# Kernel tuning notes

Measured on AMD Instinct MI355X. Metric: run time of the kernel, lower is better.

The kernel has to match this reference:

```python
import jax, jax.numpy as jnp
import numpy as np

EPS = 1e-12  # matches torch F.normalize eps

def _l2norm(x, axis):
    n = jnp.sqrt(jnp.sum(x * x, axis=axis, keepdims=True))
    return x / jnp.maximum(n, EPS)

def setup_inputs() -> dict:
    key = jax.random.key(0)
    k1, k2, k3, k4 = jax.random.split(key, 4)
    b, n_way, k_shot, q, c, h, w = 2, 5, 5, 75, 64, 21, 21
    return {
        "support_xf": jax.random.normal(k1, (b, n_way * k_shot, c, h, w), dtype=jnp.float32),
        "support_y": jax.random.randint(k2, (b, n_way * k_shot), 0, n_way),
        "query_xf": jax.random.normal(k3, (b, q, c, h, w), dtype=jnp.float32),
        "query_y": jax.random.randint(k4, (b, q), 0, n_way),
        "n_way": n_way,
        "k_shot": k_shot,
    }

def reference(support_xf, support_y, query_xf, query_y, n_way, k_shot):
    b, q, c, h, w = query_xf.shape
    hw = h * w
    # k_shot averaging: (b, n_way, k_shot, c, h, w) -> mean over shots -> (b, n_way, c, hw)
    sup = support_xf.reshape(b, n_way, k_shot, c, hw).mean(axis=2)
    qry = query_xf.reshape(b, q, c, hw)
    # cosine similarity: L2-normalize each local descriptor along channel dim
    sup_n = _l2norm(sup, axis=2)  # (b, n_way, c, hw_s)
    qry_n = _l2norm(qry, axis=2)  # (b, q, c, hw_q)
    # inner product matrix: (b, q, n_way, hw_q, hw_s)
    sim = jnp.einsum('bqcm,bwcn->bqwmn', qry_n, sup_n)
    # topk with k=1 along support descriptors, mean over k == max
    topv = jnp.max(sim, axis=-1)  # (b, q, n_way, hw_q)
    logits = topv.sum(axis=-1).reshape(b * q, n_way)  # image-to-class score
    return logits
```

## Files before the change

### kernel.cpp

```cpp
#include <hip/hip_runtime.h>
#include <hip/hip_bf16.h>

namespace {
constexpr int kB = 2, kW = 5, kS = 5, kQ = 75, kC = 64, kHW = 441;
constexpr int kNP = 448;
constexpr int kMP = 448;
constexpr int kCHUNK = 112;
constexpr int kLDT = 65;
constexpr int kTiles = kB * kQ * kW;
constexpr int kThreads = 448;
constexpr int kWaves = 7;
constexpr int kPrepGrid = 8 * 81;

typedef short bf16x8 __attribute__((ext_vector_type(8)));
typedef float f32x16 __attribute__((ext_vector_type(16)));
typedef __attribute__((address_space(3))) unsigned int lds_u32;
typedef const __attribute__((address_space(1))) unsigned int gbl_u32;
}

__global__ __launch_bounds__(256) void prep_k(const float* __restrict__ sup,
                                              const float* __restrict__ qry,
                                              unsigned short* __restrict__ snT,
                                              unsigned short* __restrict__ qnT) {
  __shared__ float img_t[kCHUNK * kLDT];
  __shared__ float inv[kCHUNK];
  const int tid = threadIdx.x;
  const int x = blockIdx.x & 7;
  const int j = blockIdx.x >> 3;

  const int start0 = (x < 6) ? 94 * x : 564 + 93 * (x - 6);
  const int start1 = (x + 1 < 6) ? 94 * (x + 1) : 564 + 93 * (x + 1 - 6);
  const int lo = (start0 + 4) / 5, hi = (start1 + 4) / 5;
  const int cnt = hi - lo;
  const int nq = 4 * cnt;

  bool is_sup;
  int bw = 0, bq = 0, chunk;
  if (j < nq) {
    is_sup = false;
    bq = lo + (j >> 2);
    chunk = j & 3;
  } else {
    int js = j - nq;
    if (js >= 5) return;
    is_sup = true;
    int u = x + 8 * js;
    bw = u >> 2;
    chunk = u & 3;
  }

  const int m0 = chunk * kCHUNK;
  const int mcnt = min(kCHUNK, kHW - m0);
  unsigned short* dst;

  if (is_sup) {
    const float* base = sup + (size_t)bw * kS * kC * kHW;
    for (int i = tid; i < kC * kCHUNK; i += 256) {
      int c = i / kCHUNK, mm = i % kCHUNK;
      float v = 0.f;
      if (mm < mcnt) {
        const float* p = base + (size_t)c * kHW + m0 + mm;
        float s = 0.f;
#pragma unroll
        for (int k = 0; k < kS; ++k) s += p[(size_t)k * kC * kHW];
        v = s * (1.f / kS);
      }
      img_t[mm * kLDT + c] = v;
    }
    dst = snT + (size_t)bw * kNP * kC;
  } else {
    const float* base = qry + (size_t)bq * kC * kHW;
    for (int i = tid; i < kC * kCHUNK; i += 256) {
      int c = i / kCHUNK, mm = i % kCHUNK;
      img_t[mm * kLDT + c] = (mm < mcnt) ? base[(size_t)c * kHW + m0 + mm] : 0.f;
    }
    dst = qnT + (size_t)bq * kMP * kC;
  }
  __syncthreads();

  if (tid < kCHUNK) {
    float ss = 0.f;
#pragma unroll
    for (int c = 0; c < kC; ++c) { float v = img_t[tid * kLDT + c]; ss += v * v; }
    inv[tid] = 1.f / fmaxf(sqrtf(ss), 1e-12f);
  }
  __syncthreads();

  for (int i8 = tid; i8 < kCHUNK * 8; i8 += 256) {
    int m = i8 >> 3, c8 = (i8 & 7) * 8;
    float sc = inv[m];
    union { unsigned short u[8]; uint4 v; } pk;
#pragma unroll
    for (int jj = 0; jj < 8; ++jj) {
      __hip_bfloat16 o = __float2bfloat16(img_t[m * kLDT + c8 + jj] * sc);
      pk.u[jj] = *reinterpret_cast<unsigned short*>(&o);
    }
    *reinterpret_cast<uint4*>(dst + ((size_t)(m0 + m) * kC + c8)) = pk.v;
  }
}

__device__ __forceinline__ float max16_v(const f32x16& a) {
  float m0 = fmaxf(fmaxf(a[0], a[1]), a[2]);
  float m1 = fmaxf(fmaxf(a[3], a[4]), a[5]);
  float m2 = fmaxf(fmaxf(a[6], a[7]), a[8]);
  float m3 = fmaxf(fmaxf(a[9], a[10]), a[11]);
  float m4 = fmaxf(fmaxf(a[12], a[13]), a[14]);
  return fmaxf(fmaxf(fmaxf(m0, m1), m2), fmaxf(fmaxf(m3, m4), a[15]));
}
__device__ __forceinline__ float max12_v(const f32x16& a) {
  float m0 = fmaxf(fmaxf(a[0], a[1]), a[2]);
  float m1 = fmaxf(fmaxf(a[3], a[4]), a[5]);
  float m2 = fmaxf(fmaxf(a[6], a[7]), a[8]);
  float m3 = fmaxf(fmaxf(a[9], a[10]), a[11]);
  return fmaxf(fmaxf(m0, m1), fmaxf(m2, m3));
}

__global__ __launch_bounds__(kThreads) void dn4_main_k(const unsigned short* __restrict__ qnT,
                                                       const unsigned short* __restrict__ snT,
                                                       float* __restrict__ out) {
  __shared__ __align__(16) unsigned short As[kNP * kC];
  __shared__ float part[kWaves];
  const int tid = threadIdx.x;

  const int xcd = blockIdx.x & 7, jj = blockIdx.x >> 3;
  const int idx = (xcd < 6) ? xcd * 94 + jj : 564 + (xcd - 6) * 93 + jj;

  const int w = idx % kW;
  const int bq = idx / kW;
  const int b = bq / kQ;

  const int lane = tid & 63;
  const int lh = lane >> 5;
  const int lm = lane & 31;
  const int wid = tid >> 6;
  const int ct0 = wid * 2;

  const unsigned short* sb = snT + (size_t)(b * kW + w) * kNP * kC;
  const unsigned short* qb = qnT + (size_t)bq * kMP * kC;
  const char* sbase = (const char*)sb;

  bf16x8 bf[2][4];
#pragma unroll
  for (int ct = 0; ct < 2; ++ct) {
    int m = (ct0 + ct) * 32 + lm;
#pragma unroll
    for (int kk = 0; kk < 4; ++kk)
      bf[ct][kk] = *reinterpret_cast<const bf16x8*>(qb + (size_t)m * kC + kk * 16 + lh * 8);
  }

#pragma unroll
  for (int it = 0; it < 8; ++it) {
    int L = it * kThreads + tid;
    int srcj = (L & ~7) | ((L & 7) ^ ((L >> 3) & 7));
    __builtin_amdgcn_global_load_lds((gbl_u32*)(sbase + ((size_t)srcj << 4)),
                                     (lds_u32*)((char*)As + ((size_t)L << 4)), 16, 0, 0);
  }

  f32x16 z;
#pragma unroll
  for (int r = 0; r < 16; ++r) z[r] = 0.f;
  float rm[2] = {-INFINITY, -INFINITY};

  asm volatile("s_waitcnt vmcnt(4)" ::: "memory");
  __builtin_amdgcn_sched_barrier(0);
  __builtin_amdgcn_s_barrier();

#pragma unroll 1
  for (int nt = 0; nt < 7; ++nt) {
    bf16x8 af[4];
    int n = nt * 32 + lm;
#pragma unroll
    for (int kk = 0; kk < 4; ++kk) {
      int k16 = kk * 2 + lh;
      af[kk] = *reinterpret_cast<const bf16x8*>(As + ((size_t)(n * 8 + (k16 ^ (n & 7))) << 3));
    }
#pragma unroll
    for (int ct = 0; ct < 2; ++ct) {
      f32x16 acc = z;
#pragma unroll
      for (int kk = 0; kk < 4; ++kk)
        acc = __builtin_amdgcn_mfma_f32_32x32x16_bf16(af[kk], bf[ct][kk], acc, 0, 0, 0);
      rm[ct] = fmaxf(rm[ct], max16_v(acc));
    }
  }

  asm volatile("s_waitcnt vmcnt(0)" ::: "memory");
  __builtin_amdgcn_sched_barrier(0);
  __builtin_amdgcn_s_barrier();

#pragma unroll 1
  for (int nt = 7; nt < 13; ++nt) {
    bf16x8 af[4];
    int n = nt * 32 + lm;
#pragma unroll
    for (int kk = 0; kk < 4; ++kk) {
      int k16 = kk * 2 + lh;
      af[kk] = *reinterpret_cast<const bf16x8*>(As + ((size_t)(n * 8 + (k16 ^ (n & 7))) << 3));
    }
#pragma unroll
    for (int ct = 0; ct < 2; ++ct) {
      f32x16 acc = z;
#pragma unroll
      for (int kk = 0; kk < 4; ++kk)
        acc = __builtin_amdgcn_mfma_f32_32x32x16_bf16(af[kk], bf[ct][kk], acc, 0, 0, 0);
      rm[ct] = fmaxf(rm[ct], max16_v(acc));
    }
  }

  {
    bf16x8 af[4];
    int n = 13 * 32 + lm;
#pragma unroll
    for (int kk = 0; kk < 4; ++kk) {
      int k16 = kk * 2 + lh;
      af[kk] = *reinterpret_cast<const bf16x8*>(As + ((size_t)(n * 8 + (k16 ^ (n & 7))) << 3));
    }
#pragma unroll
    for (int ct = 0; ct < 2; ++ct) {
      f32x16 acc = z;
#pragma unroll
      for (int kk = 0; kk < 4; ++kk)
        acc = __builtin_amdgcn_mfma_f32_32x32x16_bf16(af[kk], bf[ct][kk], acc, 0, 0, 0);
      float t = max12_v(acc);
      if (lh == 0) t = fmaxf(t, acc[12]);
      rm[ct] = fmaxf(rm[ct], t);
    }
  }

  float s = fmaxf(rm[0], __shfl_xor(rm[0], 32, 64)) +
            fmaxf(rm[1], __shfl_xor(rm[1], 32, 64));
#pragma unroll
  for (int off = 1; off < 32; off <<= 1) s += __shfl_xor(s, off, 64);

  if (lane == 0) part[wid] = s;
  __syncthreads();
  if (tid == 0) {
    float t = 0.f;
#pragma unroll
    for (int v = 0; v < kWaves; ++v) t += part[v];
    out[idx] = t;
  }
}

extern "C" void kernel_launch(void* const* d_in, const int* in_sizes, int n_in,
                              void* d_out, int out_size, void* d_ws, size_t ws_size,
                              hipStream_t stream) {
  const float* sup = (const float*)d_in[0];
  const float* qry = (const float*)d_in[2];
  float* out = (float*)d_out;

  unsigned short* snT = (unsigned short*)d_ws;
  unsigned short* qnT = snT + (size_t)kB * kW * kNP * kC;

  prep_k<<<kPrepGrid, 256, 0, stream>>>(sup, qry, snT, qnT);
  dn4_main_k<<<kTiles, kThreads, 0, stream>>>(qnT, snT, out);
}
```

Measured before the change: 38.63 us.

## Use persistent 512-block grid with double-buffered LDS halves for the main kernel

The main kernel moves from one block per (query, way) tile (750 blocks) to a fixed 512-block grid. Some blocks process two tiles, chosen by an XCD-aware rank mapping. Support staging is split into two 224-row halves held in a double-buffered LDS array, and the next half (or the next tile's first half) is prefetched while the current half is computed. The aim is to cut the tail effect of the second wave of blocks and to overlap global-to-LDS loads with MFMA work. In exchange it adds barriers and imbalance, since blocks that handle two tiles set the critical path.

```diff
diff --git a/kernel.cpp b/kernel.cpp
--- a/kernel.cpp
+++ b/kernel.cpp
@@ -10,6 +10,7 @@
 constexpr int kTiles = kB * kQ * kW;
 constexpr int kThreads = 448;
 constexpr int kWaves = 7;
+constexpr int kGrid = 512;
 constexpr int kPrepGrid = 8 * 81;
 
 typedef short bf16x8 __attribute__((ext_vector_type(8)));
@@ -31,8 +32,7 @@
   const int start0 = (x < 6) ? 94 * x : 564 + 93 * (x - 6);
   const int start1 = (x + 1 < 6) ? 94 * (x + 1) : 564 + 93 * (x + 1 - 6);
   const int lo = (start0 + 4) / 5, hi = (start1 + 4) / 5;
-  const int cnt = hi - lo;
-  const int nq = 4 * cnt;
+  const int nq = 4 * (hi - lo);
 
   bool is_sup;
   int bw = 0, bq = 0, chunk;
@@ -115,19 +115,81 @@
   return fmaxf(fmaxf(m0, m1), fmaxf(m2, m3));
 }
 
+__device__ __forceinline__ void stage_half(const unsigned short* sb, int h,
+                                           unsigned short* dstbuf, int tid) {
+  const char* sbase = (const char*)sb + (size_t)h * 1792 * 16;
+#pragma unroll
+  for (int it = 0; it < 4; ++it) {
+    int L = it * kThreads + tid;
+    int srcj = (L & ~7) | ((L & 7) ^ ((L >> 3) & 7));
+    __builtin_amdgcn_global_load_lds((gbl_u32*)(sbase + ((size_t)srcj << 4)),
+                                     (lds_u32*)((char*)dstbuf + ((size_t)L << 4)), 16, 0, 0);
+  }
+}
+
+template <bool TAIL>
+__device__ __forceinline__ void compute_half7(const unsigned short* As,
+                                              const bf16x8 bf[2][4],
+                                              int lane, float rm[2]) {
+  const int lh = lane >> 5;
+  const int lm = lane & 31;
+  const unsigned short* p0 = As + ((size_t)(lm * 8 + ((0 * 2 + lh) ^ (lm & 7))) << 3);
+  const unsigned short* p1 = As + ((size_t)(lm * 8 + ((1 * 2 + lh) ^ (lm & 7))) << 3);
+  const unsigned short* p2 = As + ((size_t)(lm * 8 + ((2 * 2 + lh) ^ (lm & 7))) << 3);
+  const unsigned short* p3 = As + ((size_t)(lm * 8 + ((3 * 2 + lh) ^ (lm & 7))) << 3);
+  f32x16 z;
+#pragma unroll
+  for (int r = 0; r < 16; ++r) z[r] = 0.f;
+
+#pragma unroll 1
+  for (int sub = 0; sub < 7; ++sub) {
+    const size_t so = (size_t)sub * 32 * kC;
+    bf16x8 af[4];
+    af[0] = *reinterpret_cast<const bf16x8*>(p0 + so);
+    af[1] = *reinterpret_cast<const bf16x8*>(p1 + so);
+    af[2] = *reinterpret_cast<const bf16x8*>(p2 + so);
+    af[3] = *reinterpret_cast<const bf16x8*>(p3 + so);
+    if (!TAIL || sub < 6) {
+#pragma unroll
+      for (int ct = 0; ct < 2; ++ct) {
+        f32x16 acc = z;
+#pragma unroll
+        for (int kk = 0; kk < 4; ++kk)
+          acc = __builtin_amdgcn_mfma_f32_32x32x16_bf16(af[kk], bf[ct][kk], acc, 0, 0, 0);
+        rm[ct] = fmaxf(rm[ct], max16_v(acc));
+      }
+    } else {
+#pragma unroll
+      for (int ct = 0; ct < 2; ++ct) {
+        f32x16 acc = z;
+#pragma unroll
+        for (int kk = 0; kk < 4; ++kk)
+          acc = __builtin_amdgcn_mfma_f32_32x32x16_bf16(af[kk], bf[ct][kk], acc, 0, 0, 0);
+        float t = max12_v(acc);
+        if (lh == 0) t = fmaxf(t, acc[12]);
+        rm[ct] = fmaxf(rm[ct], t);
+      }
+    }
+  }
+}
+
 __global__ __launch_bounds__(kThreads) void dn4_main_k(const unsigned short* __restrict__ qnT,
                                                        const unsigned short* __restrict__ snT,
                                                        float* __restrict__ out) {
-  __shared__ __align__(16) unsigned short As[kNP * kC];
+  __shared__ __align__(16) unsigned short As[2][224 * kC];
   __shared__ float part[kWaves];
   const int tid = threadIdx.x;
 
-  const int xcd = blockIdx.x & 7, jj = blockIdx.x >> 3;
-  const int idx = (xcd < 6) ? xcd * 94 + jj : 564 + (xcd - 6) * 93 + jj;
-
-  const int w = idx % kW;
-  const int bq = idx / kW;
-  const int b = bq / kQ;
+  const int xcd = blockIdx.x & 7;
+  const int s = blockIdx.x >> 3;
+  const int cnt = (xcd < 6) ? 94 : 93;
+  const int base = (xcd < 6) ? 94 * xcd : 564 + 93 * (xcd - 6);
+  const int idx0 = base + s;
+  const int rank = (s < 32) ? ((s & 1) ? (s >> 1) : -1)
+                            : (((s & 1) == 0) ? 16 + ((s - 32) >> 1) : -1);
+  const bool has2 = (rank >= 0) && (64 + rank < cnt);
+  const int idx1 = has2 ? base + 64 + rank : idx0;
+  const int P = has2 ? 4 : 2;
 
   const int lane = tid & 63;
   const int lh = lane >> 5;
@@ -135,9 +197,9 @@
   const int wid = tid >> 6;
   const int ct0 = wid * 2;
 
-  const unsigned short* sb = snT + (size_t)(b * kW + w) * kNP * kC;
-  const unsigned short* qb = qnT + (size_t)bq * kMP * kC;
-  const char* sbase = (const char*)sb;
+  const unsigned short* sb0 =
+      snT + (size_t)((idx0 / (kQ * kW)) * kW + (idx0 % kW)) * kNP * kC;
+  const unsigned short* qb0 = qnT + (size_t)(idx0 / kW) * kMP * kC;
 
   bf16x8 bf[2][4];
 #pragma unroll
@@ -145,100 +207,64 @@
     int m = (ct0 + ct) * 32 + lm;
 #pragma unroll
     for (int kk = 0; kk < 4; ++kk)
-      bf[ct][kk] = *reinterpret_cast<const bf16x8*>(qb + (size_t)m * kC + kk * 16 + lh * 8);
-  }
-
-#pragma unroll
-  for (int it = 0; it < 8; ++it) {
-    int L = it * kThreads + tid;
-    int srcj = (L & ~7) | ((L & 7) ^ ((L >> 3) & 7));
-    __builtin_amdgcn_global_load_lds((gbl_u32*)(sbase + ((size_t)srcj << 4)),
-                                     (lds_u32*)((char*)As + ((size_t)L << 4)), 16, 0, 0);
-  }
-
-  f32x16 z;
-#pragma unroll
-  for (int r = 0; r < 16; ++r) z[r] = 0.f;
+      bf[ct][kk] = *reinterpret_cast<const bf16x8*>(qb0 + (size_t)m * kC + kk * 16 + lh * 8);
+  }
+  stage_half(sb0, 0, As[0], tid);
+
   float rm[2] = {-INFINITY, -INFINITY};
 
-  asm volatile("s_waitcnt vmcnt(4)" ::: "memory");
-  __builtin_amdgcn_sched_barrier(0);
-  __builtin_amdgcn_s_barrier();
-
 #pragma unroll 1
-  for (int nt = 0; nt < 7; ++nt) {
-    bf16x8 af[4];
-    int n = nt * 32 + lm;
-#pragma unroll
-    for (int kk = 0; kk < 4; ++kk) {
-      int k16 = kk * 2 + lh;
-      af[kk] = *reinterpret_cast<const bf16x8*>(As + ((size_t)(n * 8 + (k16 ^ (n & 7))) << 3));
-    }
-#pragma unroll
-    for (int ct = 0; ct < 2; ++ct) {
-      f32x16 acc = z;
-#pragma unroll
-      for (int kk = 0; kk < 4; ++kk)
-        acc = __builtin_amdgcn_mfma_f32_32x32x16_bf16(af[kk], bf[ct][kk], acc, 0, 0, 0);
-      rm[ct] = fmaxf(rm[ct], max16_v(acc));
-    }
-  }
-
-  asm volatile("s_waitcnt vmcnt(0)" ::: "memory");
-  __builtin_amdgcn_sched_barrier(0);
-  __builtin_amdgcn_s_barrier();
-
-#pragma unroll 1
-  for (int nt = 7; nt < 13; ++nt) {
-    bf16x8 af[4];
-    int n = nt * 32 + lm;
-#pragma unroll
-    for (int kk = 0; kk < 4; ++kk) {
-      int k16 = kk * 2 + lh;
-      af[kk] = *reinterpret_cast<const bf16x8*>(As + ((size_t)(n * 8 + (k16 ^ (n & 7))) << 3));
-    }
-#pragma unroll
-    for (int ct = 0; ct < 2; ++ct) {
-      f32x16 acc = z;
-#pragma unroll
-      for (int kk = 0; kk < 4; ++kk)
-        acc = __builtin_amdgcn_mfma_f32_32x32x16_bf16(af[kk], bf[ct][kk], acc, 0, 0, 0);
-      rm[ct] = fmaxf(rm[ct], max16_v(acc));
-    }
-  }
-
-  {
-    bf16x8 af[4];
-    int n = 13 * 32 + lm;
-#pragma unroll
-    for (int kk = 0; kk < 4; ++kk) {
-      int k16 = kk * 2 + lh;
-      af[kk] = *reinterpret_cast<const bf16x8*>(As + ((size_t)(n * 8 + (k16 ^ (n & 7))) << 3));
-    }
-#pragma unroll
-    for (int ct = 0; ct < 2; ++ct) {
-      f32x16 acc = z;
-#pragma unroll
-      for (int kk = 0; kk < 4; ++kk)
-        acc = __builtin_amdgcn_mfma_f32_32x32x16_bf16(af[kk], bf[ct][kk], acc, 0, 0, 0);
-      float t = max12_v(acc);
-      if (lh == 0) t = fmaxf(t, acc[12]);
-      rm[ct] = fmaxf(rm[ct], t);
-    }
-  }
-
-  float s = fmaxf(rm[0], __shfl_xor(rm[0], 32, 64)) +
-            fmaxf(rm[1], __shfl_xor(rm[1], 32, 64));
-#pragma unroll
-  for (int off = 1; off < 32; off <<= 1) s += __shfl_xor(s, off, 64);
-
-  if (lane == 0) part[wid] = s;
-  __syncthreads();
-  if (tid == 0) {
-    float t = 0.f;
-#pragma unroll
-    for (int v = 0; v < kWaves; ++v) t += part[v];
-    out[idx] = t;
+  for (int ph = 0; ph < P; ++ph) {
+    const int cur = ph & 1;
+    const int idx = (ph >> 1) ? idx1 : idx0;
+
+    if (ph == 2) {
+      const unsigned short* qb1 = qnT + (size_t)(idx1 / kW) * kMP * kC;
+#pragma unroll
+      for (int ct = 0; ct < 2; ++ct) {
+        int m = (ct0 + ct) * 32 + lm;
+#pragma unroll
+        for (int kk = 0; kk < 4; ++kk)
+          bf[ct][kk] = *reinterpret_cast<const bf16x8*>(qb1 + (size_t)m * kC + kk * 16 + lh * 8);
+      }
+    }
+
+    if (ph + 1 < P) {
+      const int nidx = ((ph + 1) >> 1) ? idx1 : idx0;
+      const unsigned short* sbn =
+          snT + (size_t)((nidx / (kQ * kW)) * kW + (nidx % kW)) * kNP * kC;
+      stage_half(sbn, (ph + 1) & 1, As[cur ^ 1], tid);
+      asm volatile("s_waitcnt vmcnt(4)" ::: "memory");
+    } else {
+      asm volatile("s_waitcnt vmcnt(0)" ::: "memory");
+    }
+    __builtin_amdgcn_sched_barrier(0);
+    __builtin_amdgcn_s_barrier();
+    __builtin_amdgcn_sched_barrier(0);
+
+    if ((ph & 1) == 0) {
+      compute_half7<false>(As[cur], bf, lane, rm);
+      __builtin_amdgcn_s_barrier();
+      __builtin_amdgcn_sched_barrier(0);
+    } else {
+      compute_half7<true>(As[cur], bf, lane, rm);
+      float sm = fmaxf(rm[0], __shfl_xor(rm[0], 32, 64)) +
+                 fmaxf(rm[1], __shfl_xor(rm[1], 32, 64));
+#pragma unroll
+      for (int off = 1; off < 32; off <<= 1) sm += __shfl_xor(sm, off, 64);
+      if (lane == 0) part[wid] = sm;
+      asm volatile("s_waitcnt lgkmcnt(0)" ::: "memory");
+      __builtin_amdgcn_sched_barrier(0);
+      __builtin_amdgcn_s_barrier();
+      __builtin_amdgcn_sched_barrier(0);
+      if (tid == 0) {
+        float t = 0.f;
+#pragma unroll
+        for (int v = 0; v < kWaves; ++v) t += part[v];
+        out[idx] = t;
+      }
+      rm[0] = -INFINITY; rm[1] = -INFINITY;
+    }
   }
 }
 
@@ -253,5 +279,5 @@
   unsigned short* qnT = snT + (size_t)kB * kW * kNP * kC;
 
   prep_k<<<kPrepGrid, 256, 0, stream>>>(sup, qry, snT, qnT);
-  dn4_main_k<<<kTiles, kThreads, 0, stream>>>(qnT, snT, out);
-}
+  dn4_main_k<<<kGrid, kThreads, 0, stream>>>(qnT, snT, out);
+}
```

Result: slower. 39.87 us (+3.2%).

## Share one support tile in LDS across four queries per block

Applied to the files above, without the earlier changes.

The main kernel is restructured so each block loads one support class image into LDS once and has four queries read it, two waves per query, instead of one block per query-class pair. This cuts redundant support loads into LDS and the block count from 750 to 190. Each wave now holds 7 query tiles in registers (28 bf16x8 fragments), which raises register pressure. The split-phase wait that overlapped the LDS fill with early compute is replaced by a full barrier, and 190 blocks may underfill the GPU's CUs.

```diff
diff --git a/kernel.cpp b/kernel.cpp
--- a/kernel.cpp
+++ b/kernel.cpp
@@ -7,10 +7,9 @@
 constexpr int kMP = 448;
 constexpr int kCHUNK = 112;
 constexpr int kLDT = 65;
-constexpr int kTiles = kB * kQ * kW;
-constexpr int kThreads = 448;
-constexpr int kWaves = 7;
 constexpr int kPrepGrid = 8 * 81;
+constexpr int kSPerBW = 19;
+constexpr int kGrid = kB * kW * kSPerBW;
 
 typedef short bf16x8 __attribute__((ext_vector_type(8)));
 typedef float f32x16 __attribute__((ext_vector_type(16)));
@@ -31,8 +30,7 @@
   const int start0 = (x < 6) ? 94 * x : 564 + 93 * (x - 6);
   const int start1 = (x + 1 < 6) ? 94 * (x + 1) : 564 + 93 * (x + 1 - 6);
   const int lo = (start0 + 4) / 5, hi = (start1 + 4) / 5;
-  const int cnt = hi - lo;
-  const int nq = 4 * cnt;
+  const int nq = 4 * (hi - lo);
 
   bool is_sup;
   int bw = 0, bq = 0, chunk;
@@ -115,58 +113,59 @@
   return fmaxf(fmaxf(m0, m1), fmaxf(m2, m3));
 }
 
-__global__ __launch_bounds__(kThreads) void dn4_main_k(const unsigned short* __restrict__ qnT,
-                                                       const unsigned short* __restrict__ snT,
-                                                       float* __restrict__ out) {
+__global__ __launch_bounds__(512) void dn4_main_k(const unsigned short* __restrict__ qnT,
+                                                  const unsigned short* __restrict__ snT,
+                                                  float* __restrict__ out) {
   __shared__ __align__(16) unsigned short As[kNP * kC];
-  __shared__ float part[kWaves];
+  __shared__ float part[8];
   const int tid = threadIdx.x;
-
-  const int xcd = blockIdx.x & 7, jj = blockIdx.x >> 3;
-  const int idx = (xcd < 6) ? xcd * 94 + jj : 564 + (xcd - 6) * 93 + jj;
-
-  const int w = idx % kW;
-  const int bq = idx / kW;
-  const int b = bq / kQ;
+  const int bid = blockIdx.x;
+
+  const int bw = bid / kSPerBW;
+  const int s = bid % kSPerBW;
+  const int b = bw / kW;
 
   const int lane = tid & 63;
   const int lh = lane >> 5;
   const int lm = lane & 31;
   const int wid = tid >> 6;
-  const int ct0 = wid * 2;
-
-  const unsigned short* sb = snT + (size_t)(b * kW + w) * kNP * kC;
-  const unsigned short* qb = qnT + (size_t)bq * kMP * kC;
+  const int qi = wid >> 1;
+  const int wp = wid & 1;
+  const int q = s * 4 + qi;
+  const bool valid = q < kQ;
+
+  const unsigned short* sb = snT + (size_t)bw * kNP * kC;
   const char* sbase = (const char*)sb;
 
-  bf16x8 bf[2][4];
-#pragma unroll
-  for (int ct = 0; ct < 2; ++ct) {
-    int m = (ct0 + ct) * 32 + lm;
-#pragma unroll
-    for (int kk = 0; kk < 4; ++kk)
-      bf[ct][kk] = *reinterpret_cast<const bf16x8*>(qb + (size_t)m * kC + kk * 16 + lh * 8);
-  }
-
-#pragma unroll
-  for (int it = 0; it < 8; ++it) {
-    int L = it * kThreads + tid;
+  bf16x8 bf[7][4];
+  if (valid) {
+    const unsigned short* qb = qnT + (size_t)(b * kQ + q) * kMP * kC;
+#pragma unroll
+    for (int ct = 0; ct < 7; ++ct) {
+      int m = (wp * 7 + ct) * 32 + lm;
+#pragma unroll
+      for (int kk = 0; kk < 4; ++kk)
+        bf[ct][kk] = *reinterpret_cast<const bf16x8*>(qb + (size_t)m * kC + kk * 16 + lh * 8);
+    }
+  }
+
+#pragma unroll
+  for (int it = 0; it < 7; ++it) {
+    int L = it * 512 + tid;
     int srcj = (L & ~7) | ((L & 7) ^ ((L >> 3) & 7));
     __builtin_amdgcn_global_load_lds((gbl_u32*)(sbase + ((size_t)srcj << 4)),
                                      (lds_u32*)((char*)As + ((size_t)L << 4)), 16, 0, 0);
   }
-
+  __syncthreads();
+
+  float rm[7] = {-INFINITY, -INFINITY, -INFINITY, -INFINITY,
+                 -INFINITY, -INFINITY, -INFINITY};
   f32x16 z;
 #pragma unroll
   for (int r = 0; r < 16; ++r) z[r] = 0.f;
-  float rm[2] = {-INFINITY, -INFINITY};
-
-  asm volatile("s_waitcnt vmcnt(4)" ::: "memory");
-  __builtin_amdgcn_sched_barrier(0);
-  __builtin_amdgcn_s_barrier();
 
 #pragma unroll 1
-  for (int nt = 0; nt < 7; ++nt) {
+  for (int nt = 0; nt < 13; ++nt) {
     bf16x8 af[4];
     int n = nt * 32 + lm;
 #pragma unroll
@@ -174,71 +173,55 @@
       int k16 = kk * 2 + lh;
       af[kk] = *reinterpret_cast<const bf16x8*>(As + ((size_t)(n * 8 + (k16 ^ (n & 7))) << 3));
     }
-#pragma unroll
-    for (int ct = 0; ct < 2; ++ct) {
-      f32x16 acc = z;
-#pragma unroll
-      for (int kk = 0; kk < 4; ++kk)
-        acc = __builtin_amdgcn_mfma_f32_32x32x16_bf16(af[kk], bf[ct][kk], acc, 0, 0, 0);
-      rm[ct] = fmaxf(rm[ct], max16_v(acc));
-    }
-  }
-
-  asm volatile("s_waitcnt vmcnt(0)" ::: "memory");
-  __builtin_amdgcn_sched_barrier(0);
-  __builtin_amdgcn_s_barrier();
-
-#pragma unroll 1
-  for (int nt = 7; nt < 13; ++nt) {
+    if (valid) {
+#pragma unroll
+      for (int ct = 0; ct < 7; ++ct) {
+        f32x16 acc = z;
+#pragma unroll
+        for (int kk = 0; kk < 4; ++kk)
+          acc = __builtin_amdgcn_mfma_f32_32x32x16_bf16(af[kk], bf[ct][kk], acc, 0, 0, 0);
+        rm[ct] = fmaxf(rm[ct], max16_v(acc));
+      }
+    }
+  }
+
+  {
     bf16x8 af[4];
-    int n = nt * 32 + lm;
+    int n = 13 * 32 + lm;
 #pragma unroll
     for (int kk = 0; kk < 4; ++kk) {
       int k16 = kk * 2 + lh;
       af[kk] = *reinterpret_cast<const bf16x8*>(As + ((size_t)(n * 8 + (k16 ^ (n & 7))) << 3));
     }
-#pragma unroll
-    for (int ct = 0; ct < 2; ++ct) {
-      f32x16 acc = z;
-#pragma unroll
-      for (int kk = 0; kk < 4; ++kk)
-        acc = __builtin_amdgcn_mfma_f32_32x32x16_bf16(af[kk], bf[ct][kk], acc, 0, 0, 0);
-      rm[ct] = fmaxf(rm[ct], max16_v(acc));
-    }
-  }
-
-  {
-    bf16x8 af[4];
-    int n = 13 * 32 + lm;
-#pragma unroll
-    for (int kk = 0; kk < 4; ++kk) {
-      int k16 = kk * 2 + lh;
-      af[kk] = *reinterpret_cast<const bf16x8*>(As + ((size_t)(n * 8 + (k16 ^ (n & 7))) << 3));
-    }
-#pragma unroll
-    for (int ct = 0; ct < 2; ++ct) {
-      f32x16 acc = z;
-#pragma unroll
-      for (int kk = 0; kk < 4; ++kk)
-        acc = __builtin_amdgcn_mfma_f32_32x32x16_bf16(af[kk], bf[ct][kk], acc, 0, 0, 0);
-      float t = max12_v(acc);
-      if (lh == 0) t = fmaxf(t, acc[12]);
-      rm[ct] = fmaxf(rm[ct], t);
-    }
-  }
-
-  float s = fmaxf(rm[0], __shfl_xor(rm[0], 32, 64)) +
-            fmaxf(rm[1], __shfl_xor(rm[1], 32, 64));
-#pragma unroll
-  for (int off = 1; off < 32; off <<= 1) s += __shfl_xor(s, off, 64);
-
-  if (lane == 0) part[wid] = s;
-  __syncthreads();
-  if (tid == 0) {
-    float t = 0.f;
-#pragma unroll
-    for (int v = 0; v < kWaves; ++v) t += part[v];
-    out[idx] = t;
+    if (valid) {
+#pragma unroll
+      for (int ct = 0; ct < 7; ++ct) {
+        f32x16 acc = z;
+#pragma unroll
+        for (int kk = 0; kk < 4; ++kk)
+          acc = __builtin_amdgcn_mfma_f32_32x32x16_bf16(af[kk], bf[ct][kk], acc, 0, 0, 0);
+        float t = max12_v(acc);
+        if (lh == 0) t = fmaxf(t, acc[12]);
+        rm[ct] = fmaxf(rm[ct], t);
+      }
+    }
+  }
+
+  float ssum = 0.f;
+  if (valid) {
+#pragma unroll
+    for (int ct = 0; ct < 7; ++ct)
+      ssum += fmaxf(rm[ct], __shfl_xor(rm[ct], 32, 64));
+#pragma unroll
+    for (int off = 1; off < 32; off <<= 1) ssum += __shfl_xor(ssum, off, 64);
+  }
+  if (lane == 0) part[wid] = valid ? ssum : 0.f;
+  __syncthreads();
+
+  if (tid < 4) {
+    int qq = s * 4 + tid;
+    if (qq < kQ)
+      out[(size_t)(b * kQ + qq) * kW + (bw % kW)] = part[2 * tid] + part[2 * tid + 1];
   }
 }
 
@@ -253,5 +236,5 @@
   unsigned short* qnT = snT + (size_t)kB * kW * kNP * kC;
 
   prep_k<<<kPrepGrid, 256, 0, stream>>>(sup, qry, snT, qnT);
-  dn4_main_k<<<kTiles, kThreads, 0, stream>>>(qnT, snT, out);
-}
+  dn4_main_k<<<kGrid, 512, 0, stream>>>(qnT, snT, out);
+}
```

Result: slower. 44.01 us (+13.9%).
